# Optimization experiments

Hardware: AMD Instinct MI355X
Metric: run time of the kernel (lower is better)

Reference implementation:

```python
import jax, jax.numpy as jnp
import numpy as np

T, B, L = 8192, 8, 1024
HID, H, KV, D = 2048, 16, 8, 128
G = H // KV
EPS = 1e-6
SCALE = 1.0 / float(np.sqrt(D))


def _rms(x, w):
    # RMSNorm over last dim (head_dim), eps=1e-6
    return x * jax.lax.rsqrt(jnp.mean(x * x, axis=-1, keepdims=True) + EPS) * w


def _rot_half(x):
    h = x.shape[-1] // 2
    return jnp.concatenate([-x[..., h:], x[..., :h]], axis=-1)


def setup_inputs() -> dict:
    key = jax.random.key(0)
    ks = jax.random.split(key, 12)
    inp = {}
    inp["packed_sequence"] = jax.random.normal(ks[0], (T, HID), jnp.float32)
    # rotary embeddings: per-sample positions 0..L-1, packed
    pos = jnp.tile(jnp.arange(L), B).astype(jnp.float32)
    inv = 1.0 / (10000.0 ** (jnp.arange(0, D, 2, dtype=jnp.float32) / D))
    fr = pos[:, None] * inv[None, :]
    emb = jnp.concatenate([fr, fr], axis=-1)  # [T, D]
    inp["cos"] = jnp.cos(emb)
    inp["sin"] = jnp.sin(emb)
    # per-sample causal float mask (additive): 0 allowed, -1e9 masked
    tril = jnp.tril(jnp.ones((L, L), bool))
    inp["attention_mask"] = jnp.broadcast_to(
        jnp.where(tril, 0.0, -1e9).astype(jnp.float32)[None], (B, L, L)
    )
    # disjoint und/gen routing indexes covering all T tokens
    inp["und_idx"] = jnp.arange(0, T, 2, dtype=jnp.int32)
    inp["gen_idx"] = jnp.arange(1, T, 2, dtype=jnp.int32)
    s = 0.02

    def lin(k, o, i):
        return jax.random.normal(k, (o, i), jnp.float32) * s

    kk = jax.random.split(ks[1], 8)
    inp["Wq_u"] = lin(kk[0], H * D, HID); inp["bq_u"] = jnp.zeros((H * D,), jnp.float32)
    inp["Wk_u"] = lin(kk[1], KV * D, HID); inp["bk_u"] = jnp.zeros((KV * D,), jnp.float32)
    inp["Wv_u"] = lin(kk[2], KV * D, HID); inp["bv_u"] = jnp.zeros((KV * D,), jnp.float32)
    inp["Wo_u"] = lin(kk[3], HID, H * D)
    inp["Wq_g"] = lin(kk[4], H * D, HID); inp["bq_g"] = jnp.zeros((H * D,), jnp.float32)
    inp["Wk_g"] = lin(kk[5], KV * D, HID); inp["bk_g"] = jnp.zeros((KV * D,), jnp.float32)
    inp["Wv_g"] = lin(kk[6], KV * D, HID); inp["bv_g"] = jnp.zeros((KV * D,), jnp.float32)
    inp["Wo_g"] = lin(kk[7], HID, H * D)
    inp["qn_u"] = jnp.ones((D,), jnp.float32); inp["kn_u"] = jnp.ones((D,), jnp.float32)
    inp["qn_g"] = jnp.ones((D,), jnp.float32); inp["kn_g"] = jnp.ones((D,), jnp.float32)
    return inp


def reference(packed_sequence, cos, sin, attention_mask, und_idx, gen_idx,
              Wq_u, bq_u, Wk_u, bk_u, Wv_u, bv_u, Wo_u,
              Wq_g, bq_g, Wk_g, bk_g, Wv_g, bv_g, Wo_g,
              qn_u, kn_u, qn_g, kn_g):
    x_u = packed_sequence[und_idx]  # [T/2, HID]
    x_g = packed_sequence[gen_idx]

    def route(Wu, bu, Wg, bg, width):
        out = jnp.zeros((T, width), packed_sequence.dtype)
        out = out.at[und_idx].set(x_u @ Wu.T + bu)
        out = out.at[gen_idx].set(x_g @ Wg.T + bg)
        return out

    q = route(Wq_u, bq_u, Wq_g, bq_g, H * D).reshape(T, H, D)
    k = route(Wk_u, bk_u, Wk_g, bk_g, KV * D).reshape(T, KV, D)
    v = route(Wv_u, bv_u, Wv_g, bv_g, KV * D).reshape(T, KV, D)

    # routed per-head QK RMSNorm (separate und/gen weights)
    qn = jnp.zeros_like(q).at[und_idx].set(_rms(q[und_idx], qn_u)).at[gen_idx].set(_rms(q[gen_idx], qn_g))
    kn = jnp.zeros_like(k).at[und_idx].set(_rms(k[und_idx], kn_u)).at[gen_idx].set(_rms(k[gen_idx], kn_g))

    c, s = cos[:, None, :], sin[:, None, :]  # unsqueeze_dim=1
    q = qn * c + _rot_half(qn) * s
    k = kn * c + _rot_half(kn) * s

    # GQA expansion: kv head i -> heads i*G..i*G+G-1
    k = jnp.repeat(k, G, axis=1)  # [T, H, D]
    v = jnp.repeat(v, G, axis=1)

    qb = q.reshape(B, L, H, D)
    kb = k.reshape(B, L, H, D)
    vb = v.reshape(B, L, H, D)

    scores = jnp.einsum('blhd,bmhd->bhlm', qb, kb) * SCALE
    scores = scores + attention_mask[:, None, :, :]
    p = jax.nn.softmax(scores, axis=-1)
    o = jnp.einsum('bhlm,bmhd->blhd', p, vb).reshape(T, H * D)

    out = jnp.zeros((T, HID), packed_sequence.dtype)
    out = out.at[und_idx].set(o[und_idx] @ Wo_u.T)
    out = out.at[gen_idx].set(o[gen_idx] @ Wo_g.T)
    return out
```

## Files before the change

### kernel.cpp

```cpp
#include <hip/hip_runtime.h>
#include <hip/hip_bf16.h>
#include <stdint.h>
#include <math.h>

#define T_TOK 8192
#define HID   2048
#define NH    16
#define NKV   8
#define HD    128
#define LSEQ  1024
#define BATCH 8
#define QKV_N 4096
#define KDIM  2048
#define NT32  64
#define SCALE 0.08838834764831845f

typedef __hip_bfloat16 bf16;
typedef __bf16 bf16x8 __attribute__((ext_vector_type(8)));
typedef float  f32x4  __attribute__((ext_vector_type(4)));

typedef const void __attribute__((address_space(1)))* gas_ptr;
typedef void       __attribute__((address_space(3)))* las_ptr;

__device__ __forceinline__ float b2f(bf16 x) { return __bfloat162float(x); }
__device__ __forceinline__ bf16  f2b(float x) { return __float2bfloat16(x); }
__device__ __forceinline__ unsigned short f2u(float x) {
    union { bf16 b; unsigned short u; } c; c.b = __float2bfloat16(x); return c.u;
}

__device__ __forceinline__ bf16x8 ld16(const void* p) {
    union { uint4 u; bf16x8 v; } c;
    c.u = *reinterpret_cast<const uint4*>(p);
    return c.v;
}

__device__ __forceinline__ void cp16(void* lds, const void* g) {
    __builtin_amdgcn_global_load_lds((gas_ptr)g, (las_ptr)lds, 16, 0, 0);
}

#define DSR(dst, base, imm) \
    asm volatile("ds_read_b128 %0, %1 offset:" #imm : "=v"(dst) : "v"(base))
#define SCHEDB() __builtin_amdgcn_sched_barrier(0)
#define LGKM(n)  asm volatile("s_waitcnt lgkmcnt(" #n ")")

__global__ __launch_bounds__(256) void k_f2b(const float* __restrict__ in,
                                             bf16* __restrict__ out, int n) {
    int i = blockIdx.x * blockDim.x + threadIdx.x;
    int stride = gridDim.x * blockDim.x;
    const float4* in4 = (const float4*)in;
    ushort4* out4 = (ushort4*)out;
    int n4 = n >> 2;
    for (int j = i; j < n4; j += stride) {
        float4 v = in4[j];
        ushort4 o;
        o.x = f2u(v.x); o.y = f2u(v.y); o.z = f2u(v.z); o.w = f2u(v.w);
        out4[j] = o;
    }
}

__global__ __launch_bounds__(256) void k_mod(const int* __restrict__ und,
                                             const int* __restrict__ gen,
                                             int* __restrict__ mod, int n) {
    int i = blockIdx.x * blockDim.x + threadIdx.x;
    if (i < n) { mod[und[i]] = 0; mod[gen[i]] = 1; }
}

template<int EPI>
__global__ __launch_bounds__(512)
void k_gemm8p(const bf16* __restrict__ A,
              const bf16* __restrict__ Bw_u, const bf16* __restrict__ Bw_g,
              const int* __restrict__ und, const int* __restrict__ gen,
              const float* __restrict__ bq_u, const float* __restrict__ bk_u,
              const float* __restrict__ bv_u,
              const float* __restrict__ bq_g, const float* __restrict__ bk_g,
              const float* __restrict__ bv_g,
              bf16* __restrict__ outB, float* __restrict__ outF) {
    extern __shared__ char smem[];

    int modg = blockIdx.y;
    const bf16* Bw = modg ? Bw_g : Bw_u;
    const int* idx = modg ? gen : und;
    const float* bq = modg ? bq_g : bq_u;
    const float* bk = modg ? bk_g : bk_u;
    const float* bv = modg ? bv_g : bv_u;

    int gx = gridDim.x;
    int bid = blockIdx.x;
    int sw = (bid & 7) * (gx >> 3) + (bid >> 3);
    int tn = sw >> 4, tm = sw & 15;

    int tid = threadIdx.x;
    int w = tid >> 6, lane = tid & 63;
    int l16 = lane & 15, l4 = lane >> 4;
    int wm = w >> 2, wn = w & 3;

    int chunk = (lane & 3) ^ ((lane >> 3) & 3);
    const bf16* pS[2][2];
#pragma unroll
    for (int j = 0; j < 2; ++j) {
        int R = (j * 8 + w) * 16 + (lane >> 2);
        pS[0][j] = A + (size_t)idx[tm * 256 + R] * KDIM + chunk * 8;
        pS[1][j] = Bw + (size_t)(tn * 256 + R) * KDIM + chunk * 8;
    }

    auto STAGE = [&](int t) {
        char* base = smem + (t & 1) * 32768 + w * 1024;
        cp16(base,                 pS[0][0] + t * 32);
        cp16(base + 8192,          pS[0][1] + t * 32);
        cp16(base + 16384,         pS[1][0] + t * 32);
        cp16(base + 16384 + 8192,  pS[1][1] + t * 32);
    };

    f32x4 acc[8][4];
#pragma unroll
    for (int m = 0; m < 8; ++m)
#pragma unroll
        for (int n = 0; n < 4; ++n) acc[m][n] = {0.f, 0.f, 0.f, 0.f};

    STAGE(0);
    STAGE(1);

    uint32_t cByte = (uint32_t)((l4 ^ ((l16 >> 1) & 3)) << 4);
    uint32_t aOff = (uint32_t)(wm * 128 + l16) * 64 + cByte;
    uint32_t bOff = 16384u + (uint32_t)(wn * 64 + l16) * 64 + cByte;

#pragma unroll 1
    for (int t = 0; t < NT32; ++t) {
        uint32_t toff = (uint32_t)(t & 1) << 15;
        las_ptr aB = (las_ptr)(smem + toff + aOff);
        las_ptr bB = (las_ptr)(smem + toff + bOff);

        SCHEDB();
        if (t + 1 < NT32) asm volatile("s_waitcnt vmcnt(4)");
        else              asm volatile("s_waitcnt vmcnt(0)");
        __builtin_amdgcn_s_barrier();

        bf16x8 b0, b1, b2, b3, a0, a1, a2, a3, a4, a5, a6, a7;
        DSR(b0, bB, 0);    DSR(b1, bB, 1024);
        DSR(b2, bB, 2048); DSR(b3, bB, 3072);
        DSR(a0, aB, 0);    DSR(a1, aB, 1024);
        DSR(a2, aB, 2048); DSR(a3, aB, 3072);
        DSR(a4, aB, 4096); DSR(a5, aB, 5120);
        DSR(a6, aB, 6144); DSR(a7, aB, 7168);
        LGKM(4);
        SCHEDB();
        __builtin_amdgcn_s_setprio(1);
        acc[0][0] = __builtin_amdgcn_mfma_f32_16x16x32_bf16(a0, b0, acc[0][0], 0, 0, 0);
        acc[0][1] = __builtin_amdgcn_mfma_f32_16x16x32_bf16(a0, b1, acc[0][1], 0, 0, 0);
        acc[0][2] = __builtin_amdgcn_mfma_f32_16x16x32_bf16(a0, b2, acc[0][2], 0, 0, 0);
        acc[0][3] = __builtin_amdgcn_mfma_f32_16x16x32_bf16(a0, b3, acc[0][3], 0, 0, 0);
        acc[1][0] = __builtin_amdgcn_mfma_f32_16x16x32_bf16(a1, b0, acc[1][0], 0, 0, 0);
        acc[1][1] = __builtin_amdgcn_mfma_f32_16x16x32_bf16(a1, b1, acc[1][1], 0, 0, 0);
        acc[1][2] = __builtin_amdgcn_mfma_f32_16x16x32_bf16(a1, b2, acc[1][2], 0, 0, 0);
        acc[1][3] = __builtin_amdgcn_mfma_f32_16x16x32_bf16(a1, b3, acc[1][3], 0, 0, 0);
        acc[2][0] = __builtin_amdgcn_mfma_f32_16x16x32_bf16(a2, b0, acc[2][0], 0, 0, 0);
        acc[2][1] = __builtin_amdgcn_mfma_f32_16x16x32_bf16(a2, b1, acc[2][1], 0, 0, 0);
        acc[2][2] = __builtin_amdgcn_mfma_f32_16x16x32_bf16(a2, b2, acc[2][2], 0, 0, 0);
        acc[2][3] = __builtin_amdgcn_mfma_f32_16x16x32_bf16(a2, b3, acc[2][3], 0, 0, 0);
        acc[3][0] = __builtin_amdgcn_mfma_f32_16x16x32_bf16(a3, b0, acc[3][0], 0, 0, 0);
        acc[3][1] = __builtin_amdgcn_mfma_f32_16x16x32_bf16(a3, b1, acc[3][1], 0, 0, 0);
        acc[3][2] = __builtin_amdgcn_mfma_f32_16x16x32_bf16(a3, b2, acc[3][2], 0, 0, 0);
        acc[3][3] = __builtin_amdgcn_mfma_f32_16x16x32_bf16(a3, b3, acc[3][3], 0, 0, 0);
        __builtin_amdgcn_s_setprio(0);
        SCHEDB();
        LGKM(0);
        SCHEDB();
        __builtin_amdgcn_s_setprio(1);
        acc[4][0] = __builtin_amdgcn_mfma_f32_16x16x32_bf16(a4, b0, acc[4][0], 0, 0, 0);
        acc[4][1] = __builtin_amdgcn_mfma_f32_16x16x32_bf16(a4, b1, acc[4][1], 0, 0, 0);
        acc[4][2] = __builtin_amdgcn_mfma_f32_16x16x32_bf16(a4, b2, acc[4][2], 0, 0, 0);
        acc[4][3] = __builtin_amdgcn_mfma_f32_16x16x32_bf16(a4, b3, acc[4][3], 0, 0, 0);
        acc[5][0] = __builtin_amdgcn_mfma_f32_16x16x32_bf16(a5, b0, acc[5][0], 0, 0, 0);
        acc[5][1] = __builtin_amdgcn_mfma_f32_16x16x32_bf16(a5, b1, acc[5][1], 0, 0, 0);
        acc[5][2] = __builtin_amdgcn_mfma_f32_16x16x32_bf16(a5, b2, acc[5][2], 0, 0, 0);
        acc[5][3] = __builtin_amdgcn_mfma_f32_16x16x32_bf16(a5, b3, acc[5][3], 0, 0, 0);
        acc[6][0] = __builtin_amdgcn_mfma_f32_16x16x32_bf16(a6, b0, acc[6][0], 0, 0, 0);
        acc[6][1] = __builtin_amdgcn_mfma_f32_16x16x32_bf16(a6, b1, acc[6][1], 0, 0, 0);
        acc[6][2] = __builtin_amdgcn_mfma_f32_16x16x32_bf16(a6, b2, acc[6][2], 0, 0, 0);
        acc[6][3] = __builtin_amdgcn_mfma_f32_16x16x32_bf16(a6, b3, acc[6][3], 0, 0, 0);
        acc[7][0] = __builtin_amdgcn_mfma_f32_16x16x32_bf16(a7, b0, acc[7][0], 0, 0, 0);
        acc[7][1] = __builtin_amdgcn_mfma_f32_16x16x32_bf16(a7, b1, acc[7][1], 0, 0, 0);
        acc[7][2] = __builtin_amdgcn_mfma_f32_16x16x32_bf16(a7, b2, acc[7][2], 0, 0, 0);
        acc[7][3] = __builtin_amdgcn_mfma_f32_16x16x32_bf16(a7, b3, acc[7][3], 0, 0, 0);
        __builtin_amdgcn_s_setprio(0);
        SCHEDB();
        __builtin_amdgcn_s_barrier();
        if (t + 2 < NT32) STAGE(t + 2);
        SCHEDB();
    }

    int rowbase = tm * 256 + wm * 128;
    int colbase = tn * 256 + wn * 64;
#pragma unroll
    for (int m = 0; m < 8; ++m) {
#pragma unroll
        for (int r = 0; r < 4; ++r) {
            int row = rowbase + m * 16 + l4 * 4 + r;
            int token = idx[row];
#pragma unroll
            for (int n = 0; n < 4; ++n) {
                int col = colbase + n * 16 + l16;
                float v = acc[m][n][r];
                if (EPI == 0) {
                    float bias = (col < 2048) ? bq[col]
                               : (col < 3072) ? bk[col - 2048] : bv[col - 3072];
                    outB[(size_t)token * QKV_N + col] = f2b(v + bias);
                } else {
                    outF[(size_t)token * HID + col] = v;
                }
            }
        }
    }
}

__global__ __launch_bounds__(256)
void k_normrope(const bf16* __restrict__ qkv,
                const float* __restrict__ cosT, const float* __restrict__ sinT,
                const int* __restrict__ mod,
                const float* __restrict__ qn_u, const float* __restrict__ qn_g,
                const float* __restrict__ kn_u, const float* __restrict__ kn_g,
                bf16* __restrict__ Qo, bf16* __restrict__ Ko) {
    int t = blockIdx.x;
    int tid = threadIdx.x;
    int w = tid >> 6, lane = tid & 63;
    int m = mod[t];
    int b = t >> 10, pos = t & 1023;
    const bf16* row = qkv + (size_t)t * QKV_N;
    int d0 = 2 * lane, d1 = 2 * lane + 1;
    float c0 = cosT[(size_t)t * HD + d0], c1 = cosT[(size_t)t * HD + d1];
    float s0 = sinT[(size_t)t * HD + d0], s1 = sinT[(size_t)t * HD + d1];
    float sgn = (lane < 32) ? -1.f : 1.f;
    const float* qw = m ? qn_g : qn_u;
    const float* kw = m ? kn_g : kn_u;

    for (int u = w; u < 24; u += 4) {
        float v0 = b2f(row[u * HD + d0]);
        float v1 = b2f(row[u * HD + d1]);
        float ss = v0 * v0 + v1 * v1;
#pragma unroll
        for (int msk = 1; msk < 64; msk <<= 1) ss += __shfl_xor(ss, msk);
        float rs = rsqrtf(ss * (1.0f / HD) + 1e-6f);
        const float* wsc = (u < 16) ? qw : kw;
        float n0 = v0 * rs * wsc[d0], n1 = v1 * rs * wsc[d1];
        float o0 = __shfl_xor(n0, 32), o1 = __shfl_xor(n1, 32);
        float r0 = n0 * c0 + sgn * o0 * s0;
        float r1 = n1 * c1 + sgn * o1 * s1;
        if (u < 16) {
            size_t o = ((size_t)(b * NH + u) * LSEQ + pos) * HD;
            Qo[o + d0] = f2b(r0); Qo[o + d1] = f2b(r1);
        } else {
            size_t o = ((size_t)(b * NKV + (u - 16)) * LSEQ + pos) * HD;
            Ko[o + d0] = f2b(r0); Ko[o + d1] = f2b(r1);
        }
    }
}

__global__ __launch_bounds__(256)
void k_vt(const bf16* __restrict__ qkv, bf16* __restrict__ Vt) {
    __shared__ bf16 lds[64][72];
    int bk = blockIdx.x;
    int b = bk >> 3, kv = bk & 7;
    int pos0 = blockIdx.y * 64;
    int d0 = blockIdx.z * 64;
    int tid = threadIdx.x;

#pragma unroll
    for (int it = 0; it < 2; ++it) {
        int c = tid + it * 256;
        int row = c >> 3, col8 = (c & 7) * 8;
        const bf16* src = qkv + (size_t)(b * LSEQ + pos0 + row) * QKV_N
                        + 3072 + kv * HD + d0 + col8;
        *reinterpret_cast<uint4*>(&lds[row][col8]) = *reinterpret_cast<const uint4*>(src);
    }
    __syncthreads();

#pragma unroll
    for (int it = 0; it < 2; ++it) {
        int c = tid + it * 256;
        int drow = c & 63, pos8 = (c >> 6) * 8;
        union { unsigned short s[8]; uint4 u; } g;
#pragma unroll
        for (int j = 0; j < 8; ++j)
            g.s[j] = *reinterpret_cast<const unsigned short*>(&lds[pos8 + j][drow]);
        bf16* dst = Vt + ((size_t)bk * HD + d0 + drow) * LSEQ + pos0 + pos8;
        *reinterpret_cast<uint4*>(dst) = g.u;
    }
}

__global__ __launch_bounds__(256)
void k_attn(const bf16* __restrict__ Q, const bf16* __restrict__ K,
            const bf16* __restrict__ Vt, bf16* __restrict__ O) {
    int bid = blockIdx.x;
    int p = bid & 3;
    int h = (bid >> 2) & 15;
    int b = bid >> 6;
    int tid = threadIdx.x;
    int w = tid >> 6, lane = tid & 63;
    int l16 = lane & 15, l4 = lane >> 4;
    int j = p * 4 + w;

    const bf16* qhb = Q + (size_t)(b * NH + h) * LSEQ * HD;
    int kv = h >> 1;
    const bf16* kb = K + (size_t)(b * NKV + kv) * LSEQ * HD;
    const bf16* vtb = Vt + (size_t)(b * NKV + kv) * HD * LSEQ;

    __shared__ bf16 Pl[4][32][72];

    f32x4 zero = {0.f, 0.f, 0.f, 0.f};

#pragma unroll 1
    for (int half = 0; half < 2; ++half) {
        int rowblk = half ? (31 - j) : j;
        int q0 = rowblk * 32;
        int kend = q0 + 32;

        bf16x8 qf[2][4];
#pragma unroll
        for (int rf = 0; rf < 2; ++rf)
#pragma unroll
            for (int c = 0; c < 4; ++c)
                qf[rf][c] = ld16(qhb + (size_t)(q0 + rf * 16 + l16) * HD + c * 32 + l4 * 8);

        f32x4 oacc[2][8];
#pragma unroll
        for (int rf = 0; rf < 2; ++rf)
#pragma unroll
            for (int d = 0; d < 8; ++d) oacc[rf][d] = zero;
        float mr[2][4], lr[2][4];
#pragma unroll
        for (int rf = 0; rf < 2; ++rf)
#pragma unroll
            for (int r = 0; r < 4; ++r) { mr[rf][r] = -INFINITY; lr[rf][r] = 0.f; }

        for (int kt = 0; kt < kend; kt += 64) {
            f32x4 s[2][4];
#pragma unroll
            for (int rf = 0; rf < 2; ++rf)
#pragma unroll
                for (int kf = 0; kf < 4; ++kf) s[rf][kf] = zero;
#pragma unroll
            for (int c = 0; c < 4; ++c) {
                bf16x8 kf4[4];
#pragma unroll
                for (int kf = 0; kf < 4; ++kf)
                    kf4[kf] = ld16(kb + (size_t)(kt + kf * 16 + l16) * HD + c * 32 + l4 * 8);
#pragma unroll
                for (int rf = 0; rf < 2; ++rf)
#pragma unroll
                    for (int kf = 0; kf < 4; ++kf)
                        s[rf][kf] = __builtin_amdgcn_mfma_f32_16x16x32_bf16(qf[rf][c], kf4[kf], s[rf][kf], 0, 0, 0);
            }
#pragma unroll
            for (int rf = 0; rf < 2; ++rf) {
#pragma unroll
                for (int r = 0; r < 4; ++r) {
                    int qrow = q0 + rf * 16 + l4 * 4 + r;
                    float sc[4];
                    float rm = -1e30f;
#pragma unroll
                    for (int kf = 0; kf < 4; ++kf) {
                        int key = kt + kf * 16 + l16;
                        sc[kf] = (key <= qrow) ? s[rf][kf][r] * SCALE : -1e30f;
                        rm = fmaxf(rm, sc[kf]);
                    }
#pragma unroll
                    for (int msk = 1; msk < 16; msk <<= 1) rm = fmaxf(rm, __shfl_xor(rm, msk));
                    float mn = fmaxf(mr[rf][r], rm);
                    float corr = __expf(mr[rf][r] - mn);
                    mr[rf][r] = mn;
                    float rsum = 0.f;
#pragma unroll
                    for (int kf = 0; kf < 4; ++kf) {
                        float pv = __expf(sc[kf] - mn);
                        rsum += pv;
                        Pl[w][rf * 16 + l4 * 4 + r][kf * 16 + l16] = f2b(pv);
                    }
#pragma unroll
                    for (int msk = 1; msk < 16; msk <<= 1) rsum += __shfl_xor(rsum, msk);
                    lr[rf][r] = lr[rf][r] * corr + rsum;
#pragma unroll
                    for (int d = 0; d < 8; ++d) oacc[rf][d][r] *= corr;
                }
            }
            bf16x8 pf[2][2];
#pragma unroll
            for (int rf = 0; rf < 2; ++rf)
#pragma unroll
                for (int ks = 0; ks < 2; ++ks)
                    pf[rf][ks] = ld16(&Pl[w][rf * 16 + l16][ks * 32 + l4 * 8]);
#pragma unroll
            for (int dt = 0; dt < 8; ++dt) {
#pragma unroll
                for (int ks = 0; ks < 2; ++ks) {
                    bf16x8 vfr = ld16(vtb + (size_t)(dt * 16 + l16) * LSEQ + kt + ks * 32 + l4 * 8);
#pragma unroll
                    for (int rf = 0; rf < 2; ++rf)
                        oacc[rf][dt] = __builtin_amdgcn_mfma_f32_16x16x32_bf16(pf[rf][ks], vfr, oacc[rf][dt], 0, 0, 0);
                }
            }
        }

#pragma unroll
        for (int rf = 0; rf < 2; ++rf)
#pragma unroll
            for (int r = 0; r < 4; ++r) lr[rf][r] = 1.0f / lr[rf][r];
        int trow = b * LSEQ + q0;
#pragma unroll
        for (int rf = 0; rf < 2; ++rf)
#pragma unroll
            for (int dt = 0; dt < 8; ++dt)
#pragma unroll
                for (int r = 0; r < 4; ++r) {
                    int t = trow + rf * 16 + l4 * 4 + r;
                    O[(size_t)t * HID + h * HD + dt * 16 + l16] = f2b(oacc[rf][dt][r] * lr[rf][r]);
                }
    }
}

extern "C" void kernel_launch(void* const* d_in, const int* in_sizes, int n_in,
                              void* d_out, int out_size, void* d_ws, size_t ws_size,
                              hipStream_t stream) {
    const float* x    = (const float*)d_in[0];
    const float* cosT = (const float*)d_in[1];
    const float* sinT = (const float*)d_in[2];
    const int* und = (const int*)d_in[4];
    const int* gen = (const int*)d_in[5];
    const float* Wq_u = (const float*)d_in[6];
    const float* bq_u = (const float*)d_in[7];
    const float* Wk_u = (const float*)d_in[8];
    const float* bk_u = (const float*)d_in[9];
    const float* Wv_u = (const float*)d_in[10];
    const float* bv_u = (const float*)d_in[11];
    const float* Wo_u = (const float*)d_in[12];
    const float* Wq_g = (const float*)d_in[13];
    const float* bq_g = (const float*)d_in[14];
    const float* Wk_g = (const float*)d_in[15];
    const float* bk_g = (const float*)d_in[16];
    const float* Wv_g = (const float*)d_in[17];
    const float* bv_g = (const float*)d_in[18];
    const float* Wo_g = (const float*)d_in[19];
    const float* qn_u = (const float*)d_in[20];
    const float* kn_u = (const float*)d_in[21];
    const float* qn_g = (const float*)d_in[22];
    const float* kn_g = (const float*)d_in[23];
    float* out = (float*)d_out;

    char* ws = (char*)d_ws;
    size_t off = 0;
    auto alloc = [&](size_t bytes) -> void* {
        void* p = ws + off;
        off += (bytes + 255) & ~(size_t)255;
        return p;
    };
    bf16* xb      = (bf16*)alloc((size_t)T_TOK * HID * 2);
    bf16* Wqkv_u  = (bf16*)alloc((size_t)QKV_N * KDIM * 2);
    bf16* Wqkv_g  = (bf16*)alloc((size_t)QKV_N * KDIM * 2);
    bf16* Wob_u   = (bf16*)alloc((size_t)HID * HID * 2);
    bf16* Wob_g   = (bf16*)alloc((size_t)HID * HID * 2);
    int*  mod     = (int*)alloc((size_t)T_TOK * 4);
    bf16* qkv     = (bf16*)alloc((size_t)T_TOK * QKV_N * 2);
    bf16* Qa      = (bf16*)alloc((size_t)BATCH * NH  * LSEQ * HD * 2);
    bf16* Ka      = (bf16*)alloc((size_t)BATCH * NKV * LSEQ * HD * 2);
    bf16* Vt      = (bf16*)alloc((size_t)BATCH * NKV * HD * LSEQ * 2);
    bf16* Ob      = (bf16*)alloc((size_t)T_TOK * HID * 2);
    (void)ws_size; (void)in_sizes; (void)n_in; (void)out_size;

    k_f2b<<<1024, 256, 0, stream>>>(x, xb, T_TOK * HID);
    k_f2b<<<1024, 256, 0, stream>>>(Wq_u, Wqkv_u,               2048 * 2048);
    k_f2b<<<1024, 256, 0, stream>>>(Wk_u, Wqkv_u + 2048 * 2048, 1024 * 2048);
    k_f2b<<<1024, 256, 0, stream>>>(Wv_u, Wqkv_u + 3072 * 2048, 1024 * 2048);
    k_f2b<<<1024, 256, 0, stream>>>(Wq_g, Wqkv_g,               2048 * 2048);
    k_f2b<<<1024, 256, 0, stream>>>(Wk_g, Wqkv_g + 2048 * 2048, 1024 * 2048);
    k_f2b<<<1024, 256, 0, stream>>>(Wv_g, Wqkv_g + 3072 * 2048, 1024 * 2048);
    k_f2b<<<1024, 256, 0, stream>>>(Wo_u, Wob_u, 2048 * 2048);
    k_f2b<<<1024, 256, 0, stream>>>(Wo_g, Wob_g, 2048 * 2048);
    k_mod<<<16, 256, 0, stream>>>(und, gen, mod, T_TOK / 2);

    k_gemm8p<0><<<dim3(16 * 16, 2), 512, 65536, stream>>>(
        xb, Wqkv_u, Wqkv_g, und, gen, bq_u, bk_u, bv_u, bq_g, bk_g, bv_g,
        qkv, nullptr);

    k_normrope<<<T_TOK, 256, 0, stream>>>(qkv, cosT, sinT, mod,
                                          qn_u, qn_g, kn_u, kn_g, Qa, Ka);
    k_vt<<<dim3(BATCH * NKV, LSEQ / 64, HD / 64), 256, 0, stream>>>(qkv, Vt);

    k_attn<<<BATCH * NH * 4, 256, 0, stream>>>(Qa, Ka, Vt, Ob);

    k_gemm8p<1><<<dim3(8 * 16, 2), 512, 65536, stream>>>(
        Ob, Wob_u, Wob_g, und, gen, nullptr, nullptr, nullptr,
        nullptr, nullptr, nullptr, nullptr, out);
}
```

Baseline: 486.8 us.

## Deepen GEMM K-step to 64 with finer-grained staged loads across four phases

The routed GEMM kernel now processes a K-tile of 64 per iteration using 128 KB of double-buffered LDS. Each iteration is split into four MFMA phases, and each phase issues part of the next tile's global-to-LDS loads, so copies are interleaved with compute rather than issued in one burst. This is meant to halve loop overhead and hide global-load latency better. The cost is more barriers per iteration and a doubled shared-memory footprint, which limits occupancy to one block per CU.

```diff
diff --git a/kernel.cpp b/kernel.cpp
--- a/kernel.cpp
+++ b/kernel.cpp
@@ -12,7 +12,7 @@
 #define BATCH 8
 #define QKV_N 4096
 #define KDIM  2048
-#define NT32  64
+#define NT64  32
 #define SCALE 0.08838834764831845f
 
 typedef __hip_bfloat16 bf16;
@@ -41,7 +41,8 @@
 #define DSR(dst, base, imm) \
     asm volatile("ds_read_b128 %0, %1 offset:" #imm : "=v"(dst) : "v"(base))
 #define SCHEDB() __builtin_amdgcn_sched_barrier(0)
-#define LGKM(n)  asm volatile("s_waitcnt lgkmcnt(" #n ")")
+#define LGKM0()  asm volatile("s_waitcnt lgkmcnt(0)")
+#define MFMA16(a_, b_, c_) __builtin_amdgcn_mfma_f32_16x16x32_bf16(a_, b_, c_, 0, 0, 0)
 
 __global__ __launch_bounds__(256) void k_f2b(const float* __restrict__ in,
                                              bf16* __restrict__ out, int n) {
@@ -67,14 +68,14 @@
 
 template<int EPI>
 __global__ __launch_bounds__(512)
-void k_gemm8p(const bf16* __restrict__ A,
-              const bf16* __restrict__ Bw_u, const bf16* __restrict__ Bw_g,
-              const int* __restrict__ und, const int* __restrict__ gen,
-              const float* __restrict__ bq_u, const float* __restrict__ bk_u,
-              const float* __restrict__ bv_u,
-              const float* __restrict__ bq_g, const float* __restrict__ bk_g,
-              const float* __restrict__ bv_g,
-              bf16* __restrict__ outB, float* __restrict__ outF) {
+void k_g201(const bf16* __restrict__ A,
+            const bf16* __restrict__ Bw_u, const bf16* __restrict__ Bw_g,
+            const int* __restrict__ und, const int* __restrict__ gen,
+            const float* __restrict__ bq_u, const float* __restrict__ bk_u,
+            const float* __restrict__ bv_u,
+            const float* __restrict__ bq_g, const float* __restrict__ bk_g,
+            const float* __restrict__ bv_g,
+            bf16* __restrict__ outB, float* __restrict__ outF) {
     extern __shared__ char smem[];
 
     int modg = blockIdx.y;
@@ -94,21 +95,20 @@
     int l16 = lane & 15, l4 = lane >> 4;
     int wm = w >> 2, wn = w & 3;
 
-    int chunk = (lane & 3) ^ ((lane >> 3) & 3);
-    const bf16* pS[2][2];
+    int swzc = (tid & 3) ^ ((tid >> 3) & 3);
+    const bf16* pA[2]; const bf16* pB[2];
 #pragma unroll
     for (int j = 0; j < 2; ++j) {
-        int R = (j * 8 + w) * 16 + (lane >> 2);
-        pS[0][j] = A + (size_t)idx[tm * 256 + R] * KDIM + chunk * 8;
-        pS[1][j] = Bw + (size_t)(tn * 256 + R) * KDIM + chunk * 8;
-    }
-
-    auto STAGE = [&](int t) {
-        char* base = smem + (t & 1) * 32768 + w * 1024;
-        cp16(base,                 pS[0][0] + t * 32);
-        cp16(base + 8192,          pS[0][1] + t * 32);
-        cp16(base + 16384,         pS[1][0] + t * 32);
-        cp16(base + 16384 + 8192,  pS[1][1] + t * 32);
+        int row = j * 128 + (tid >> 2);
+        pA[j] = A + (size_t)idx[tm * 256 + row] * KDIM + swzc * 8;
+        pB[j] = Bw + (size_t)(tn * 256 + row) * KDIM + swzc * 8;
+    }
+
+    auto SU = [&](int t, int u, int kh) {
+        char* dest = smem + (t & 1) * 65536 + u * 32768 + kh * 16384 + w * 1024;
+        const bf16* const* p = u ? pB : pA;
+        cp16(dest,        p[0] + t * 64 + kh * 32);
+        cp16(dest + 8192, p[1] + t * 64 + kh * 32);
     };
 
     f32x4 acc[8][4];
@@ -117,77 +117,87 @@
 #pragma unroll
         for (int n = 0; n < 4; ++n) acc[m][n] = {0.f, 0.f, 0.f, 0.f};
 
-    STAGE(0);
-    STAGE(1);
+    SU(0, 0, 0); SU(0, 1, 0); SU(0, 0, 1); SU(0, 1, 1);
+    SU(1, 0, 0); SU(1, 1, 0);
+    SCHEDB();
+    asm volatile("s_waitcnt vmcnt(8)");
+    __builtin_amdgcn_s_barrier();
 
     uint32_t cByte = (uint32_t)((l4 ^ ((l16 >> 1) & 3)) << 4);
-    uint32_t aOff = (uint32_t)(wm * 128 + l16) * 64 + cByte;
-    uint32_t bOff = 16384u + (uint32_t)(wn * 64 + l16) * 64 + cByte;
+    uint32_t aBase = (uint32_t)(wm * 128 + l16) * 64 + cByte;
+    uint32_t bBase = 32768u + (uint32_t)(wn * 64 + l16) * 64 + cByte;
+
+#define MROW(MI, XV) \
+    acc[MI][0] = MFMA16(XV, b0, acc[MI][0]); \
+    acc[MI][1] = MFMA16(XV, b1, acc[MI][1]); \
+    acc[MI][2] = MFMA16(XV, b2, acc[MI][2]); \
+    acc[MI][3] = MFMA16(XV, b3, acc[MI][3]);
 
 #pragma unroll 1
-    for (int t = 0; t < NT32; ++t) {
-        uint32_t toff = (uint32_t)(t & 1) << 15;
-        las_ptr aB = (las_ptr)(smem + toff + aOff);
-        las_ptr bB = (las_ptr)(smem + toff + bOff);
-
-        SCHEDB();
-        if (t + 1 < NT32) asm volatile("s_waitcnt vmcnt(4)");
+    for (int t = 0; t < NT64; ++t) {
+        char* buf = smem + (t & 1) * 65536;
+        las_ptr aP = (las_ptr)(buf + aBase);
+        las_ptr bP = (las_ptr)(buf + bBase);
+        bf16x8 b0, b1, b2, b3, x0, x1, x2, x3;
+
+        DSR(b0, bP, 0);    DSR(b1, bP, 1024);
+        DSR(b2, bP, 2048); DSR(b3, bP, 3072);
+        DSR(x0, aP, 0);    DSR(x1, aP, 1024);
+        DSR(x2, aP, 2048); DSR(x3, aP, 3072);
+        if (t + 1 < NT64) SU(t + 1, 0, 1);
+        SCHEDB();
+        __builtin_amdgcn_s_barrier();
+        LGKM0(); SCHEDB();
+        __builtin_amdgcn_s_setprio(1);
+        MROW(0, x0) MROW(1, x1) MROW(2, x2) MROW(3, x3)
+        __builtin_amdgcn_s_setprio(0);
+        SCHEDB();
+        __builtin_amdgcn_s_barrier();
+
+        DSR(x0, aP, 4096); DSR(x1, aP, 5120);
+        DSR(x2, aP, 6144); DSR(x3, aP, 7168);
+        if (t + 1 < NT64) SU(t + 1, 1, 1);
+        SCHEDB();
+        if (t < NT64 - 1) asm volatile("s_waitcnt vmcnt(8)");
         else              asm volatile("s_waitcnt vmcnt(0)");
         __builtin_amdgcn_s_barrier();
-
-        bf16x8 b0, b1, b2, b3, a0, a1, a2, a3, a4, a5, a6, a7;
-        DSR(b0, bB, 0);    DSR(b1, bB, 1024);
-        DSR(b2, bB, 2048); DSR(b3, bB, 3072);
-        DSR(a0, aB, 0);    DSR(a1, aB, 1024);
-        DSR(a2, aB, 2048); DSR(a3, aB, 3072);
-        DSR(a4, aB, 4096); DSR(a5, aB, 5120);
-        DSR(a6, aB, 6144); DSR(a7, aB, 7168);
-        LGKM(4);
-        SCHEDB();
+        LGKM0(); SCHEDB();
         __builtin_amdgcn_s_setprio(1);
-        acc[0][0] = __builtin_amdgcn_mfma_f32_16x16x32_bf16(a0, b0, acc[0][0], 0, 0, 0);
-        acc[0][1] = __builtin_amdgcn_mfma_f32_16x16x32_bf16(a0, b1, acc[0][1], 0, 0, 0);
-        acc[0][2] = __builtin_amdgcn_mfma_f32_16x16x32_bf16(a0, b2, acc[0][2], 0, 0, 0);
-        acc[0][3] = __builtin_amdgcn_mfma_f32_16x16x32_bf16(a0, b3, acc[0][3], 0, 0, 0);
-        acc[1][0] = __builtin_amdgcn_mfma_f32_16x16x32_bf16(a1, b0, acc[1][0], 0, 0, 0);
-        acc[1][1] = __builtin_amdgcn_mfma_f32_16x16x32_bf16(a1, b1, acc[1][1], 0, 0, 0);
-        acc[1][2] = __builtin_amdgcn_mfma_f32_16x16x32_bf16(a1, b2, acc[1][2], 0, 0, 0);
-        acc[1][3] = __builtin_amdgcn_mfma_f32_16x16x32_bf16(a1, b3, acc[1][3], 0, 0, 0);
-        acc[2][0] = __builtin_amdgcn_mfma_f32_16x16x32_bf16(a2, b0, acc[2][0], 0, 0, 0);
-        acc[2][1] = __builtin_amdgcn_mfma_f32_16x16x32_bf16(a2, b1, acc[2][1], 0, 0, 0);
-        acc[2][2] = __builtin_amdgcn_mfma_f32_16x16x32_bf16(a2, b2, acc[2][2], 0, 0, 0);
-        acc[2][3] = __builtin_amdgcn_mfma_f32_16x16x32_bf16(a2, b3, acc[2][3], 0, 0, 0);
-        acc[3][0] = __builtin_amdgcn_mfma_f32_16x16x32_bf16(a3, b0, acc[3][0], 0, 0, 0);
-        acc[3][1] = __builtin_amdgcn_mfma_f32_16x16x32_bf16(a3, b1, acc[3][1], 0, 0, 0);
-        acc[3][2] = __builtin_amdgcn_mfma_f32_16x16x32_bf16(a3, b2, acc[3][2], 0, 0, 0);
-        acc[3][3] = __builtin_amdgcn_mfma_f32_16x16x32_bf16(a3, b3, acc[3][3], 0, 0, 0);
+        MROW(4, x0) MROW(5, x1) MROW(6, x2) MROW(7, x3)
         __builtin_amdgcn_s_setprio(0);
         SCHEDB();
-        LGKM(0);
-        SCHEDB();
+        __builtin_amdgcn_s_barrier();
+
+        DSR(b0, bP, 16384); DSR(b1, bP, 17408);
+        DSR(b2, bP, 18432); DSR(b3, bP, 19456);
+        DSR(x0, aP, 16384); DSR(x1, aP, 17408);
+        DSR(x2, aP, 18432); DSR(x3, aP, 19456);
+        if (t + 2 < NT64) SU(t + 2, 0, 0);
+        SCHEDB();
+        __builtin_amdgcn_s_barrier();
+        LGKM0(); SCHEDB();
         __builtin_amdgcn_s_setprio(1);
-        acc[4][0] = __builtin_amdgcn_mfma_f32_16x16x32_bf16(a4, b0, acc[4][0], 0, 0, 0);
-        acc[4][1] = __builtin_amdgcn_mfma_f32_16x16x32_bf16(a4, b1, acc[4][1], 0, 0, 0);
-        acc[4][2] = __builtin_amdgcn_mfma_f32_16x16x32_bf16(a4, b2, acc[4][2], 0, 0, 0);
-        acc[4][3] = __builtin_amdgcn_mfma_f32_16x16x32_bf16(a4, b3, acc[4][3], 0, 0, 0);
-        acc[5][0] = __builtin_amdgcn_mfma_f32_16x16x32_bf16(a5, b0, acc[5][0], 0, 0, 0);
-        acc[5][1] = __builtin_amdgcn_mfma_f32_16x16x32_bf16(a5, b1, acc[5][1], 0, 0, 0);
-        acc[5][2] = __builtin_amdgcn_mfma_f32_16x16x32_bf16(a5, b2, acc[5][2], 0, 0, 0);
-        acc[5][3] = __builtin_amdgcn_mfma_f32_16x16x32_bf16(a5, b3, acc[5][3], 0, 0, 0);
-        acc[6][0] = __builtin_amdgcn_mfma_f32_16x16x32_bf16(a6, b0, acc[6][0], 0, 0, 0);
-        acc[6][1] = __builtin_amdgcn_mfma_f32_16x16x32_bf16(a6, b1, acc[6][1], 0, 0, 0);
-        acc[6][2] = __builtin_amdgcn_mfma_f32_16x16x32_bf16(a6, b2, acc[6][2], 0, 0, 0);
-        acc[6][3] = __builtin_amdgcn_mfma_f32_16x16x32_bf16(a6, b3, acc[6][3], 0, 0, 0);
-        acc[7][0] = __builtin_amdgcn_mfma_f32_16x16x32_bf16(a7, b0, acc[7][0], 0, 0, 0);
-        acc[7][1] = __builtin_amdgcn_mfma_f32_16x16x32_bf16(a7, b1, acc[7][1], 0, 0, 0);
-        acc[7][2] = __builtin_amdgcn_mfma_f32_16x16x32_bf16(a7, b2, acc[7][2], 0, 0, 0);
-        acc[7][3] = __builtin_amdgcn_mfma_f32_16x16x32_bf16(a7, b3, acc[7][3], 0, 0, 0);
+        MROW(0, x0) MROW(1, x1) MROW(2, x2) MROW(3, x3)
         __builtin_amdgcn_s_setprio(0);
         SCHEDB();
         __builtin_amdgcn_s_barrier();
-        if (t + 2 < NT32) STAGE(t + 2);
-        SCHEDB();
-    }
+
+        DSR(x0, aP, 20480); DSR(x1, aP, 21504);
+        DSR(x2, aP, 22528); DSR(x3, aP, 23552);
+        if (t + 2 < NT64) SU(t + 2, 1, 0);
+        SCHEDB();
+        if (t < NT64 - 2)       asm volatile("s_waitcnt vmcnt(8)");
+        else if (t == NT64 - 2) asm volatile("s_waitcnt vmcnt(4)");
+        else                    asm volatile("s_waitcnt vmcnt(0)");
+        __builtin_amdgcn_s_barrier();
+        LGKM0(); SCHEDB();
+        __builtin_amdgcn_s_setprio(1);
+        MROW(4, x0) MROW(5, x1) MROW(6, x2) MROW(7, x3)
+        __builtin_amdgcn_s_setprio(0);
+        SCHEDB();
+        __builtin_amdgcn_s_barrier();
+    }
+#undef MROW
 
     int rowbase = tm * 256 + wm * 128;
     int colbase = tn * 256 + wn * 64;
@@ -348,7 +358,7 @@
                 for (int rf = 0; rf < 2; ++rf)
 #pragma unroll
                     for (int kf = 0; kf < 4; ++kf)
-                        s[rf][kf] = __builtin_amdgcn_mfma_f32_16x16x32_bf16(qf[rf][c], kf4[kf], s[rf][kf], 0, 0, 0);
+                        s[rf][kf] = MFMA16(qf[rf][c], kf4[kf], s[rf][kf]);
             }
 #pragma unroll
             for (int rf = 0; rf < 2; ++rf) {
@@ -395,7 +405,7 @@
                     bf16x8 vfr = ld16(vtb + (size_t)(dt * 16 + l16) * LSEQ + kt + ks * 32 + l4 * 8);
 #pragma unroll
                     for (int rf = 0; rf < 2; ++rf)
-                        oacc[rf][dt] = __builtin_amdgcn_mfma_f32_16x16x32_bf16(pf[rf][ks], vfr, oacc[rf][dt], 0, 0, 0);
+                        oacc[rf][dt] = MFMA16(pf[rf][ks], vfr, oacc[rf][dt]);
                 }
             }
         }
@@ -465,6 +475,11 @@
     bf16* Ob      = (bf16*)alloc((size_t)T_TOK * HID * 2);
     (void)ws_size; (void)in_sizes; (void)n_in; (void)out_size;
 
+    (void)hipFuncSetAttribute((const void*)k_g201<0>,
+                              hipFuncAttributeMaxDynamicSharedMemorySize, 131072);
+    (void)hipFuncSetAttribute((const void*)k_g201<1>,
+                              hipFuncAttributeMaxDynamicSharedMemorySize, 131072);
+
     k_f2b<<<1024, 256, 0, stream>>>(x, xb, T_TOK * HID);
     k_f2b<<<1024, 256, 0, stream>>>(Wq_u, Wqkv_u,               2048 * 2048);
     k_f2b<<<1024, 256, 0, stream>>>(Wk_u, Wqkv_u + 2048 * 2048, 1024 * 2048);
@@ -476,7 +491,7 @@
     k_f2b<<<1024, 256, 0, stream>>>(Wo_g, Wob_g, 2048 * 2048);
     k_mod<<<16, 256, 0, stream>>>(und, gen, mod, T_TOK / 2);
 
-    k_gemm8p<0><<<dim3(16 * 16, 2), 512, 65536, stream>>>(
+    k_g201<0><<<dim3(16 * 16, 2), 512, 131072, stream>>>(
         xb, Wqkv_u, Wqkv_g, und, gen, bq_u, bk_u, bv_u, bq_g, bk_g, bv_g,
         qkv, nullptr);
 
@@ -486,7 +501,7 @@
 
     k_attn<<<BATCH * NH * 4, 256, 0, stream>>>(Qa, Ka, Vt, Ob);
 
-    k_gemm8p<1><<<dim3(8 * 16, 2), 512, 65536, stream>>>(
+    k_g201<1><<<dim3(8 * 16, 2), 512, 131072, stream>>>(
         Ob, Wob_u, Wob_g, und, gen, nullptr, nullptr, nullptr,
         nullptr, nullptr, nullptr, nullptr, out);
 }
```

Measured after the change: 480.4 us. Within noise of the previous version (-1.3%).
